# Kernel optimization log

Hardware: AMD Instinct MI355X
Metric: run time of the kernel (lower is better)

The kernel has to match this reference:

```python
import jax, jax.numpy as jnp
import numpy as np
from jax import lax

B, C, H, W = 8, 128, 48, 48
N = H * W
SPARSITY = 0.8
K_TOP = int(N * SPARSITY)


def conv2d(x, w, b, padding, dilation=1):
    # x: [B,C,H,W], w: [O,I,kh,kw]
    out = lax.conv_general_dilated(
        x, w, window_strides=(1, 1),
        padding=[(padding, padding), (padding, padding)],
        rhs_dilation=(dilation, dilation),
        dimension_numbers=('NCHW', 'OIHW', 'NCHW'))
    return out + b[None, :, None, None]


def setup_inputs() -> dict:
    key = jax.random.key(0)
    ks = jax.random.split(key, 16)
    s = 0.02
    return {
        'x': jax.random.normal(ks[0], (B, C, H, W), jnp.float32),
        'prev_features': jax.random.normal(ks[1], (B, C, H, W), jnp.float32),
        'Wq': jax.random.normal(ks[2], (C, C), jnp.float32) * s,
        'bq': jnp.zeros((C,), jnp.float32),
        'Wk': jax.random.normal(ks[3], (C, C), jnp.float32) * s,
        'bk': jnp.zeros((C,), jnp.float32),
        'Wv': jax.random.normal(ks[4], (C, C), jnp.float32) * s,
        'bv': jnp.zeros((C,), jnp.float32),
        'ref_w': jax.random.normal(ks[5], (C, C, 3, 3), jnp.float32) * s,
        'ref_b': jnp.zeros((C,), jnp.float32),
        'gate_w': jax.random.normal(ks[6], (1, C, 3, 3), jnp.float32) * s,
        'gate_b': jnp.zeros((1,), jnp.float32),
        'cov_w': jax.random.normal(ks[7], (C, C, 3, 3), jnp.float32) * s,
        'cov_b': jnp.zeros((C,), jnp.float32),
    }


def reference(x, prev_features, Wq, bq, Wk, bk, Wv, bv,
              ref_w, ref_b, gate_w, gate_b, cov_w, cov_b):
    b_, c_, h_, w_ = x.shape
    n_ = h_ * w_
    # torch x.view(B, -1, C): raw reshape of NCHW memory (NOT a transpose)
    t = x.reshape(b_, n_, c_)
    # Linear layers (torch: y = x @ W.T + b)
    Q = t @ Wq.T + bq
    Kt = (t @ Wk.T + bk).transpose(0, 2, 1)  # [B,C,N]
    V = t @ Wv.T + bv
    attn = jnp.einsum('bnc,bcm->bnm', Q, Kt) / (c_ ** 0.5)  # [B,N,N]
    # top-k masking with scatter, as in the original
    _, idx = lax.top_k(attn, K_TOP)  # [B,N,k]
    bi = jnp.arange(b_)[:, None, None]
    ni = jnp.arange(n_)[None, :, None]
    mask = jnp.zeros_like(attn).at[bi, ni, idx].set(1.0)
    attn = attn * mask - 1e10 * (1.0 - mask)
    attn = jax.nn.softmax(attn, axis=-1)
    out = jnp.einsum('bnm,bmc->bnc', attn, V)  # [B,N,C]
    # torch view([B, C, sqrt(N), sqrt(N)]): raw reshape
    xs = out.reshape(b_, c_, h_, w_)
    # localized refinement
    importance = jax.nn.sigmoid(conv2d(xs, gate_w, gate_b, padding=1))
    xr = conv2d(xs * importance, ref_w, ref_b, padding=1)
    xs = xs + xr
    # temporal propagation
    xs = xs + 0.5 * prev_features
    # fast coverage conv: kernel 3, dilation 2, padding = 1 + 2 - 1 = 2
    return conv2d(xs, cov_w, cov_b, padding=2, dilation=2)
```

## Files before the change

kernel.cpp:

```cpp
#include <hip/hip_runtime.h>
#include <hip/hip_bf16.h>
#include <math.h>

#define BB 8
#define CC 128
#define NTOK 2304
#define KTOP 1843

typedef unsigned short u16;
typedef unsigned int   u32;
typedef __attribute__((ext_vector_type(8))) short short8;
typedef __attribute__((ext_vector_type(4))) float f32x4;

static __device__ __forceinline__ float bf2f(u16 u) {
    return __uint_as_float(((u32)u) << 16);
}
static __device__ __forceinline__ u16 f2bf(float f) {
    u32 x = __float_as_uint(f);
    return (u16)((x + 0x7fffu + ((x >> 16) & 1u)) >> 16);
}

__global__ __launch_bounds__(256) void qkv_kernel(
    const float* __restrict__ x,
    const float* __restrict__ Wq, const float* __restrict__ bq,
    const float* __restrict__ Wk, const float* __restrict__ bk,
    const float* __restrict__ Wv, const float* __restrict__ bv,
    u16* __restrict__ q_ws, u16* __restrict__ k_ws, u16* __restrict__ v_ws)
{
    __shared__ float t_lds[128 * 68];
    __shared__ u16 st[64 * 128];
    int blk = blockIdx.x;
    int b  = blk / 36;
    int n0 = (blk % 36) * 64;
    int tid = threadIdx.x;
    const float* xb = x + (size_t)(b * NTOK + n0) * CC;
    #pragma unroll
    for (int k = 0; k < 32; ++k) {
        int idx = k * 256 + tid;
        t_lds[(idx & 127) * 68 + (idx >> 7)] = xb[idx];
    }
    __syncthreads();
    int o  = tid & 127;
    int rh = tid >> 7;
    const float* Ws[3] = {Wq, Wk, Wv};
    const float* bs[3] = {bq, bk, bv};
    for (int mat = 0; mat < 3; ++mat) {
        const float* W = Ws[mat];
        float acc[32];
        #pragma unroll
        for (int j = 0; j < 32; ++j) acc[j] = 0.f;
        for (int c = 0; c < 128; ++c) {
            float w = W[o * 128 + c];
            const float4* t4p = (const float4*)&t_lds[c * 68 + rh * 32];
            #pragma unroll
            for (int j4 = 0; j4 < 8; ++j4) {
                float4 t4 = t4p[j4];
                acc[j4*4+0] += t4.x * w;
                acc[j4*4+1] += t4.y * w;
                acc[j4*4+2] += t4.z * w;
                acc[j4*4+3] += t4.w * w;
            }
        }
        float bias = bs[mat][o];
        if (mat == 2) {
            ushort4* vp4 = (ushort4*)(v_ws + (size_t)(b * CC + o) * NTOK + n0 + rh * 32);
            #pragma unroll
            for (int j8 = 0; j8 < 8; ++j8) {
                ushort4 s;
                s.x = f2bf(acc[j8*4+0] + bias); s.y = f2bf(acc[j8*4+1] + bias);
                s.z = f2bf(acc[j8*4+2] + bias); s.w = f2bf(acc[j8*4+3] + bias);
                vp4[j8] = s;
            }
        } else {
            #pragma unroll
            for (int j = 0; j < 32; ++j)
                st[(rh * 32 + j) * 128 + o] = f2bf(acc[j] + bias);
            __syncthreads();
            u16* gp = (mat == 0 ? q_ws : k_ws) + (size_t)(b * NTOK + n0) * CC;
            const ushort4* s4 = (const ushort4*)st;
            ushort4* g4 = (ushort4*)gp;
            for (int k = tid; k < 2048; k += 256) g4[k] = s4[k];
            __syncthreads();
        }
    }
}

__global__ __launch_bounds__(512) void attn_kernel(
    const u16* __restrict__ q_ws, const u16* __restrict__ k_ws,
    const u16* __restrict__ v_ws, float* __restrict__ xs_ws)
{
    __shared__ u16 sp[16 * NTOK];
    __shared__ float rowinv[16];
    int tid  = threadIdx.x;
    int lane = tid & 63, wid = tid >> 6;
    int b  = blockIdx.x & 7;
    int n0 = (blockIdx.x >> 3) * 16;
    const float scale = 0.08838834764831845f;

    int fr = lane & 15;
    int fg = lane >> 4;

    const u16* qbase = q_ws + (size_t)(b * NTOK + n0 + fr) * CC + fg * 8;
    short8 qa[4];
    #pragma unroll
    for (int kc = 0; kc < 4; ++kc)
        qa[kc] = *(const short8*)(qbase + kc * 32);

    const u16* kb = k_ws + (size_t)(b * NTOK + fr) * CC + fg * 8;
    for (int t = wid; t < 144; t += 8) {
        int m0 = t * 16;
        f32x4 acc = {0.f, 0.f, 0.f, 0.f};
        const u16* kp = kb + (size_t)m0 * CC;
        #pragma unroll
        for (int kc = 0; kc < 4; ++kc) {
            short8 kf = *(const short8*)(kp + kc * 32);
            acc = __builtin_amdgcn_mfma_f32_16x16x32_bf16(qa[kc], kf, acc, 0, 0, 0);
        }
        int mcol = m0 + fr;
        #pragma unroll
        for (int r = 0; r < 4; ++r) {
            int q = fg * 4 + r;
            sp[q * NTOK + (mcol ^ ((q & 7) << 3))] = f2bf(acc[r] * scale);
        }
    }
    __syncthreads();

    for (int rr = 0; rr < 2; ++rr) {
        int row = wid * 2 + rr;
        int xorv = (row & 7) << 3;
        u16* srow = sp + row * NTOK;
        int keys[36];
        float vmax = -1e30f;
        #pragma unroll
        for (int j = 0; j < 36; ++j) {
            int m = lane + j * 64;
            u16 raw = srow[m ^ xorv];
            u32 key = (raw & 0x8000u) ? (u32)(0xFFFFu & ~(u32)raw) : (u32)(raw | 0x8000u);
            keys[j] = (int)key;
            vmax = fmaxf(vmax, bf2f(raw));
        }
        #pragma unroll
        for (int off = 32; off; off >>= 1) vmax = fmaxf(vmax, __shfl_xor(vmax, off, 64));
        u32 res = 0;
        for (int bit = 15; bit >= 0; --bit) {
            int cand = (int)(res | (1u << bit));
            int cnt = 0;
            #pragma unroll
            for (int j = 0; j < 36; ++j) cnt += (keys[j] >= cand) ? 1 : 0;
            #pragma unroll
            for (int off = 32; off; off >>= 1) cnt += __shfl_xor(cnt, off, 64);
            if (cnt >= KTOP) res = (u32)cand;
        }
        float lsum = 0.f;
        #pragma unroll
        for (int j = 0; j < 36; ++j) {
            int m = lane + j * 64;
            float e = 0.f;
            if ((u32)keys[j] >= res) e = __expf(bf2f(srow[m ^ xorv]) - vmax);
            srow[m ^ xorv] = f2bf(e);
            lsum += e;
        }
        #pragma unroll
        for (int off = 32; off; off >>= 1) lsum += __shfl_xor(lsum, off, 64);
        if (lane == 0) rowinv[row] = 1.f / lsum;
    }
    __syncthreads();

    {
        int c0 = wid * 16;
        const u16* vb = v_ws + (size_t)(b * CC + c0 + fr) * NTOK + fg * 8;
        const u16* arow = sp + fr * NTOK;
        int xorv = (fr & 7) << 3;
        f32x4 oacc = {0.f, 0.f, 0.f, 0.f};
        for (int ch = 0; ch < 72; ++ch) {
            int m0 = ch * 32;
            short8 pa = *(const short8*)(arow + ((m0 + fg * 8) ^ xorv));
            short8 vf = *(const short8*)(vb + m0);
            oacc = __builtin_amdgcn_mfma_f32_16x16x32_bf16(pa, vf, oacc, 0, 0, 0);
        }
        #pragma unroll
        for (int r = 0; r < 4; ++r) {
            int q = fg * 4 + r;
            xs_ws[(size_t)(b * NTOK + n0 + q) * CC + c0 + fr] = oacc[r] * rowinv[q];
        }
    }
}

__global__ __launch_bounds__(256) void gate_kernel(
    const float* __restrict__ xs_ws, const float* __restrict__ gw,
    const float* __restrict__ gb, float* __restrict__ imp_ws)
{
    __shared__ float gsum[256];
    int blk = blockIdx.x;
    int b  = blk & 7;
    int p0 = (blk >> 3) * 64;
    int tid = threadIdx.x;
    int pl = tid & 63, cq = tid >> 6;
    int p = p0 + pl;
    int h = p / 48, w = p % 48;
    float acc = 0.f;
    const float* xb = xs_ws + (size_t)b * CC * NTOK;
    for (int i = cq * 32; i < cq * 32 + 32; ++i) {
        const float* plane = xb + (size_t)i * NTOK;
        const float* wv = gw + i * 9;
        #pragma unroll
        for (int kh = 0; kh < 3; ++kh) {
            int hh = h + kh - 1;
            if ((unsigned)hh >= 48u) continue;
            #pragma unroll
            for (int kw = 0; kw < 3; ++kw) {
                int ww = w + kw - 1;
                if ((unsigned)ww >= 48u) continue;
                acc += plane[hh * 48 + ww] * wv[kh * 3 + kw];
            }
        }
    }
    gsum[cq * 64 + pl] = acc;
    __syncthreads();
    if (tid < 64) {
        float s = gsum[tid] + gsum[64 + tid] + gsum[128 + tid] + gsum[192 + tid] + gb[0];
        imp_ws[b * NTOK + p0 + tid] = 1.f / (1.f + __expf(-s));
    }
}

__global__ __launch_bounds__(256) void wtrans_kernel(
    const float* __restrict__ rw, const float* __restrict__ cw,
    u16* __restrict__ wb_ref, u16* __restrict__ wb_cov)
{
    int idx = blockIdx.x * 256 + threadIdx.x;
    int which = idx >= 147456;
    int rem = which ? idx - 147456 : idx;
    int tap = rem >> 14;
    int rest = rem & 16383;
    int o = rest >> 7, c = rest & 127;
    const float* src = which ? cw : rw;
    u16* dst = which ? wb_cov : wb_ref;
    dst[rem] = f2bf(src[(o * 128 + c) * 9 + tap]);
}

__global__ __launch_bounds__(256) void tpos_kernel(
    const float* __restrict__ xs_ws, const float* __restrict__ prev,
    const float* __restrict__ imp_ws,
    u16* __restrict__ xt_g, float* __restrict__ rbuf)
{
    __shared__ float tx[128 * 65];
    __shared__ float tp[128 * 65];
    int blk = blockIdx.x;
    int b  = blk & 7;
    int p0 = (blk >> 3) * 64;
    int tid = threadIdx.x;
    const float* xsb = xs_ws + (size_t)b * CC * NTOK + p0;
    const float* pvb = prev  + (size_t)b * CC * NTOK + p0;
    #pragma unroll
    for (int it = 0; it < 32; ++it) {
        int idx = it * 256 + tid;
        int i = idx >> 6, pp = idx & 63;
        tx[i * 65 + pp] = xsb[(size_t)i * NTOK + pp];
        tp[i * 65 + pp] = pvb[(size_t)i * NTOK + pp];
    }
    __syncthreads();
    int pl = tid & 63, cq = tid >> 6;
    float impv = imp_ws[b * NTOK + p0 + pl];
    size_t obase = ((size_t)b * NTOK + p0 + pl) * CC + cq * 32;
    u16* gout = xt_g + obase;
    float* rout = rbuf + obase;
    #pragma unroll
    for (int j4 = 0; j4 < 8; ++j4) {
        float4 rv; ushort4 gv;
        float v0 = tx[(cq * 32 + j4 * 4 + 0) * 65 + pl];
        float v1 = tx[(cq * 32 + j4 * 4 + 1) * 65 + pl];
        float v2 = tx[(cq * 32 + j4 * 4 + 2) * 65 + pl];
        float v3 = tx[(cq * 32 + j4 * 4 + 3) * 65 + pl];
        float q0 = tp[(cq * 32 + j4 * 4 + 0) * 65 + pl];
        float q1 = tp[(cq * 32 + j4 * 4 + 1) * 65 + pl];
        float q2 = tp[(cq * 32 + j4 * 4 + 2) * 65 + pl];
        float q3 = tp[(cq * 32 + j4 * 4 + 3) * 65 + pl];
        rv.x = v0 + 0.5f * q0; rv.y = v1 + 0.5f * q1;
        rv.z = v2 + 0.5f * q2; rv.w = v3 + 0.5f * q3;
        gv.x = f2bf(v0 * impv); gv.y = f2bf(v1 * impv);
        gv.z = f2bf(v2 * impv); gv.w = f2bf(v3 * impv);
        *(float4*)(rout + j4 * 4) = rv;
        *(ushort4*)(gout + j4 * 4) = gv;
    }
}

__global__ __launch_bounds__(256) void refgemm_kernel(
    const u16* __restrict__ xt_g, const u16* __restrict__ wb_ref,
    const float* __restrict__ rbuf, const float* __restrict__ rb,
    u16* __restrict__ xt2)
{
    __shared__ u16 slab[144 * 128];
    int tid = threadIdx.x;
    int lane = tid & 63, wid = tid >> 6;
    int blk = blockIdx.x;
    int b  = blk & 7;
    int st = (blk >> 3) & 15;
    int oh = blk >> 7;
    int h0 = st * 3;
    int p0g = st * 144;
    int fr = lane & 15, fg = lane >> 4;
    int o0 = oh * 64 + wid * 16;
    const u16* xb = xt_g + (size_t)b * NTOK * CC;

    f32x4 acc[9];
    #pragma unroll
    for (int pt = 0; pt < 9; ++pt) acc[pt] = (f32x4){0.f, 0.f, 0.f, 0.f};

    for (int tap = 0; tap < 9; ++tap) {
        int dh = tap / 3 - 1, dw = tap % 3 - 1;
        __syncthreads();
        #pragma unroll
        for (int it = 0; it < 9; ++it) {
            int idx = it * 256 + tid;
            int pr = idx >> 4, cv = idx & 15;
            int r = pr >= 96 ? 2 : (pr >= 48 ? 1 : 0);
            int w = pr - r * 48;
            int sh = h0 + r + dh, sw = w + dw;
            short8 val = (short8){0,0,0,0,0,0,0,0};
            if ((unsigned)sh < 48u && (unsigned)sw < 48u)
                val = *(const short8*)(xb + (size_t)(sh * 48 + sw) * CC + cv * 8);
            *(short8*)(slab + pr * 128 + ((cv ^ (pr & 7)) * 8)) = val;
        }
        __syncthreads();
        #pragma unroll
        for (int kc = 0; kc < 4; ++kc) {
            short8 bfr = *(const short8*)(wb_ref + tap * 16384 + (o0 + fr) * 128 + kc * 32 + fg * 8);
            #pragma unroll
            for (int pt = 0; pt < 9; ++pt) {
                int prr = pt * 16 + fr;
                short8 pa = *(const short8*)(slab + prr * 128 + (((kc * 4 + fg) ^ (prr & 7)) * 8));
                acc[pt] = __builtin_amdgcn_mfma_f32_16x16x32_bf16(pa, bfr, acc[pt], 0, 0, 0);
            }
        }
    }
    int o = o0 + fr;
    float bias = rb[o];
    #pragma unroll
    for (int pt = 0; pt < 9; ++pt) {
        #pragma unroll
        for (int r = 0; r < 4; ++r) {
            int p = p0g + pt * 16 + fg * 4 + r;
            size_t off = ((size_t)b * NTOK + p) * CC + o;
            float v = acc[pt][r] + bias + rbuf[off];
            xt2[off] = f2bf(v);
        }
    }
}

__global__ __launch_bounds__(256) void covgemm_kernel(
    const u16* __restrict__ xt2, const u16* __restrict__ wb_cov,
    const float* __restrict__ cb, float* __restrict__ out)
{
    __shared__ u16 slab[144 * 128];
    __shared__ float ldsout[4 * 16 * 145];
    int tid = threadIdx.x;
    int lane = tid & 63, wid = tid >> 6;
    int blk = blockIdx.x;
    int b  = blk & 7;
    int st = (blk >> 3) & 15;
    int oh = blk >> 7;
    int h0 = st * 3;
    int p0g = st * 144;
    int fr = lane & 15, fg = lane >> 4;
    int o0 = oh * 64 + wid * 16;
    const u16* xb = xt2 + (size_t)b * NTOK * CC;

    f32x4 acc[9];
    #pragma unroll
    for (int pt = 0; pt < 9; ++pt) acc[pt] = (f32x4){0.f, 0.f, 0.f, 0.f};

    for (int tap = 0; tap < 9; ++tap) {
        int dh = (tap / 3 - 1) * 2, dw = (tap % 3 - 1) * 2;
        __syncthreads();
        #pragma unroll
        for (int it = 0; it < 9; ++it) {
            int idx = it * 256 + tid;
            int pr = idx >> 4, cv = idx & 15;
            int r = pr >= 96 ? 2 : (pr >= 48 ? 1 : 0);
            int w = pr - r * 48;
            int sh = h0 + r + dh, sw = w + dw;
            short8 val = (short8){0,0,0,0,0,0,0,0};
            if ((unsigned)sh < 48u && (unsigned)sw < 48u)
                val = *(const short8*)(xb + (size_t)(sh * 48 + sw) * CC + cv * 8);
            *(short8*)(slab + pr * 128 + ((cv ^ (pr & 7)) * 8)) = val;
        }
        __syncthreads();
        #pragma unroll
        for (int kc = 0; kc < 4; ++kc) {
            short8 bfr = *(const short8*)(wb_cov + tap * 16384 + (o0 + fr) * 128 + kc * 32 + fg * 8);
            #pragma unroll
            for (int pt = 0; pt < 9; ++pt) {
                int prr = pt * 16 + fr;
                short8 pa = *(const short8*)(slab + prr * 128 + (((kc * 4 + fg) ^ (prr & 7)) * 8));
                acc[pt] = __builtin_amdgcn_mfma_f32_16x16x32_bf16(pa, bfr, acc[pt], 0, 0, 0);
            }
        }
    }
    float bias = cb[o0 + fr];
    float* lo = ldsout + wid * (16 * 145);
    #pragma unroll
    for (int pt = 0; pt < 9; ++pt) {
        #pragma unroll
        for (int r = 0; r < 4; ++r) {
            int pl = pt * 16 + fg * 4 + r;
            lo[fr * 145 + pl] = acc[pt][r] + bias;
        }
    }
    __syncthreads();
    float* ob = out + ((size_t)b * CC + o0) * NTOK + p0g;
    #pragma unroll
    for (int j = 0; j < 36; ++j) {
        int idx = j * 64 + lane;
        int o_r = idx / 144;
        int p_r = idx - o_r * 144;
        ob[(size_t)o_r * NTOK + p_r] = lo[o_r * 145 + p_r];
    }
}

extern "C" void kernel_launch(void* const* d_in, const int* in_sizes, int n_in,
                              void* d_out, int out_size, void* d_ws, size_t ws_size,
                              hipStream_t stream)
{
    const float* x    = (const float*)d_in[0];
    const float* prev = (const float*)d_in[1];
    const float* Wq   = (const float*)d_in[2];
    const float* bq   = (const float*)d_in[3];
    const float* Wk   = (const float*)d_in[4];
    const float* bk   = (const float*)d_in[5];
    const float* Wv   = (const float*)d_in[6];
    const float* bv   = (const float*)d_in[7];
    const float* rw   = (const float*)d_in[8];
    const float* rb   = (const float*)d_in[9];
    const float* gw   = (const float*)d_in[10];
    const float* gb   = (const float*)d_in[11];
    const float* cw   = (const float*)d_in[12];
    const float* cb   = (const float*)d_in[13];
    float* out = (float*)d_out;
    char* ws = (char*)d_ws;

    const size_t SZ  = (size_t)BB * NTOK * CC;
    const size_t BSZ = SZ * 2;
    const size_t FSZ = SZ * 4;
    u16*   q_ws   = (u16*)(ws);
    u16*   k_ws   = (u16*)(ws + BSZ);
    u16*   v_ws   = (u16*)(ws + 2 * BSZ);
    float* xs_ws  = (float*)(ws + 3 * BSZ);
    float* imp_ws = (float*)(ws + 3 * BSZ + FSZ);
    u16*   xt_g   = (u16*)(ws + 3 * BSZ + FSZ + 73728);
    float* rbuf   = (float*)(ws + 4 * BSZ + FSZ + 73728);
    u16*   xt2    = (u16*)(ws + 4 * BSZ + 2 * FSZ + 73728);
    u16*   wb_ref = (u16*)(ws + 5 * BSZ + 2 * FSZ + 73728);
    u16*   wb_cov = (u16*)(ws + 5 * BSZ + 2 * FSZ + 73728 + 294912);

    qkv_kernel<<<dim3(288), dim3(256), 0, stream>>>(x, Wq, bq, Wk, bk, Wv, bv,
                                                    q_ws, k_ws, v_ws);
    attn_kernel<<<dim3(1152), dim3(512), 0, stream>>>(q_ws, k_ws, v_ws, xs_ws);
    gate_kernel<<<dim3(288), dim3(256), 0, stream>>>(xs_ws, gw, gb, imp_ws);
    wtrans_kernel<<<dim3(1152), dim3(256), 0, stream>>>(rw, cw, wb_ref, wb_cov);
    tpos_kernel<<<dim3(288), dim3(256), 0, stream>>>(xs_ws, prev, imp_ws, xt_g, rbuf);
    refgemm_kernel<<<dim3(256), dim3(256), 0, stream>>>(xt_g, wb_ref, rbuf, rb, xt2);
    covgemm_kernel<<<dim3(256), dim3(256), 0, stream>>>(xt2, wb_cov, cb, out);
}
```

Before: 586.5 us.

## Shrink attention tiles to 8 query rows, store sort keys, fold scale into Q

Attention blocks now cover 8 query rows with 4 waves instead of 16 rows with 8 waves, halving shared memory per block and doubling the grid. Score tiles are stored directly as monotone sort keys so the top-k pass needs no conversion, and the max is taken on keys. The softmax scale is folded into Q in the QKV kernel. Each wave handles two rows at once for ILP and two V column tiles per MFMA loop. The cost is that half of each 16-row MFMA output is wasted on duplicate rows.

Result: slower. 656.2 us (+11.9%).

```diff
diff --git a/kernel.cpp b/kernel.cpp
--- a/kernel.cpp
+++ b/kernel.cpp
@@ -18,6 +18,10 @@
 static __device__ __forceinline__ u16 f2bf(float f) {
     u32 x = __float_as_uint(f);
     return (u16)((x + 0x7fffu + ((x >> 16) & 1u)) >> 16);
+}
+static __device__ __forceinline__ float key2val(int k) {
+    u32 raw = (k & 0x8000) ? (u32)(k ^ 0x8000) : ((~(u32)k) & 0xFFFFu);
+    return __uint_as_float(raw << 16);
 }
 
 __global__ __launch_bounds__(256) void qkv_kernel(
@@ -72,9 +76,10 @@
                 vp4[j8] = s;
             }
         } else {
+            float sc = (mat == 0) ? 0.08838834764831845f : 1.0f;
             #pragma unroll
             for (int j = 0; j < 32; ++j)
-                st[(rh * 32 + j) * 128 + o] = f2bf(acc[j] + bias);
+                st[(rh * 32 + j) * 128 + o] = f2bf((acc[j] + bias) * sc);
             __syncthreads();
             u16* gp = (mat == 0 ? q_ws : k_ws) + (size_t)(b * NTOK + n0) * CC;
             const ushort4* s4 = (const ushort4*)st;
@@ -85,29 +90,27 @@
     }
 }
 
-__global__ __launch_bounds__(512) void attn_kernel(
+__global__ __launch_bounds__(256) void attn_kernel(
     const u16* __restrict__ q_ws, const u16* __restrict__ k_ws,
     const u16* __restrict__ v_ws, float* __restrict__ xs_ws)
 {
-    __shared__ u16 sp[16 * NTOK];
-    __shared__ float rowinv[16];
+    __shared__ u16 sp[8 * NTOK];
+    __shared__ float rowinv[8];
     int tid  = threadIdx.x;
     int lane = tid & 63, wid = tid >> 6;
     int b  = blockIdx.x & 7;
-    int n0 = (blockIdx.x >> 3) * 16;
-    const float scale = 0.08838834764831845f;
-
+    int n0 = (blockIdx.x >> 3) * 8;
     int fr = lane & 15;
     int fg = lane >> 4;
 
-    const u16* qbase = q_ws + (size_t)(b * NTOK + n0 + fr) * CC + fg * 8;
+    const u16* qbase = q_ws + (size_t)(b * NTOK + n0 + (fr & 7)) * CC + fg * 8;
     short8 qa[4];
     #pragma unroll
     for (int kc = 0; kc < 4; ++kc)
         qa[kc] = *(const short8*)(qbase + kc * 32);
 
     const u16* kb = k_ws + (size_t)(b * NTOK + fr) * CC + fg * 8;
-    for (int t = wid; t < 144; t += 8) {
+    for (int t = wid; t < 144; t += 4) {
         int m0 = t * 16;
         f32x4 acc = {0.f, 0.f, 0.f, 0.f};
         const u16* kp = kb + (size_t)m0 * CC;
@@ -116,72 +119,106 @@
             short8 kf = *(const short8*)(kp + kc * 32);
             acc = __builtin_amdgcn_mfma_f32_16x16x32_bf16(qa[kc], kf, acc, 0, 0, 0);
         }
-        int mcol = m0 + fr;
-        #pragma unroll
-        for (int r = 0; r < 4; ++r) {
-            int q = fg * 4 + r;
-            sp[q * NTOK + (mcol ^ ((q & 7) << 3))] = f2bf(acc[r] * scale);
+        if (fg < 2) {
+            int mcol = m0 + fr;
+            #pragma unroll
+            for (int r = 0; r < 4; ++r) {
+                int q = fg * 4 + r;
+                u16 raw = f2bf(acc[r]);
+                u16 key = (raw & 0x8000u) ? (u16)~raw : (u16)(raw | 0x8000u);
+                sp[q * NTOK + (mcol ^ ((q & 7) << 3))] = key;
+            }
         }
     }
     __syncthreads();
 
-    for (int rr = 0; rr < 2; ++rr) {
-        int row = wid * 2 + rr;
-        int xorv = (row & 7) << 3;
-        u16* srow = sp + row * NTOK;
-        int keys[36];
-        float vmax = -1e30f;
+    {
+        int row0 = wid * 2, row1 = row0 + 1;
+        int x0 = (row0 & 7) << 3, x1 = (row1 & 7) << 3;
+        u16* s0 = sp + row0 * NTOK;
+        u16* s1 = sp + row1 * NTOK;
+        int keys0[36], keys1[36];
+        int kmax0 = 0, kmax1 = 0;
         #pragma unroll
         for (int j = 0; j < 36; ++j) {
             int m = lane + j * 64;
-            u16 raw = srow[m ^ xorv];
-            u32 key = (raw & 0x8000u) ? (u32)(0xFFFFu & ~(u32)raw) : (u32)(raw | 0x8000u);
-            keys[j] = (int)key;
-            vmax = fmaxf(vmax, bf2f(raw));
-        }
-        #pragma unroll
-        for (int off = 32; off; off >>= 1) vmax = fmaxf(vmax, __shfl_xor(vmax, off, 64));
-        u32 res = 0;
+            int k0 = s0[m ^ x0];
+            int k1 = s1[m ^ x1];
+            keys0[j] = k0; keys1[j] = k1;
+            kmax0 = max(kmax0, k0); kmax1 = max(kmax1, k1);
+        }
+        #pragma unroll
+        for (int off = 32; off; off >>= 1) {
+            kmax0 = max(kmax0, __shfl_xor(kmax0, off, 64));
+            kmax1 = max(kmax1, __shfl_xor(kmax1, off, 64));
+        }
+        u32 res0 = 0, res1 = 0;
         for (int bit = 15; bit >= 0; --bit) {
-            int cand = (int)(res | (1u << bit));
-            int cnt = 0;
-            #pragma unroll
-            for (int j = 0; j < 36; ++j) cnt += (keys[j] >= cand) ? 1 : 0;
-            #pragma unroll
-            for (int off = 32; off; off >>= 1) cnt += __shfl_xor(cnt, off, 64);
-            if (cnt >= KTOP) res = (u32)cand;
-        }
-        float lsum = 0.f;
+            int cand0 = (int)(res0 | (1u << bit));
+            int cand1 = (int)(res1 | (1u << bit));
+            int c0 = 0, c1 = 0;
+            #pragma unroll
+            for (int j = 0; j < 36; ++j) {
+                c0 += (keys0[j] >= cand0) ? 1 : 0;
+                c1 += (keys1[j] >= cand1) ? 1 : 0;
+            }
+            #pragma unroll
+            for (int off = 32; off; off >>= 1) {
+                c0 += __shfl_xor(c0, off, 64);
+                c1 += __shfl_xor(c1, off, 64);
+            }
+            if (c0 >= KTOP) res0 = (u32)cand0;
+            if (c1 >= KTOP) res1 = (u32)cand1;
+        }
+        float vmax0 = key2val(kmax0), vmax1 = key2val(kmax1);
+        float sum0 = 0.f, sum1 = 0.f;
         #pragma unroll
         for (int j = 0; j < 36; ++j) {
             int m = lane + j * 64;
-            float e = 0.f;
-            if ((u32)keys[j] >= res) e = __expf(bf2f(srow[m ^ xorv]) - vmax);
-            srow[m ^ xorv] = f2bf(e);
-            lsum += e;
-        }
-        #pragma unroll
-        for (int off = 32; off; off >>= 1) lsum += __shfl_xor(lsum, off, 64);
-        if (lane == 0) rowinv[row] = 1.f / lsum;
+            float e0 = 0.f, e1 = 0.f;
+            if ((u32)keys0[j] >= res0) e0 = __expf(key2val(keys0[j]) - vmax0);
+            if ((u32)keys1[j] >= res1) e1 = __expf(key2val(keys1[j]) - vmax1);
+            s0[m ^ x0] = f2bf(e0);
+            s1[m ^ x1] = f2bf(e1);
+            sum0 += e0; sum1 += e1;
+        }
+        #pragma unroll
+        for (int off = 32; off; off >>= 1) {
+            sum0 += __shfl_xor(sum0, off, 64);
+            sum1 += __shfl_xor(sum1, off, 64);
+        }
+        if (lane == 0) {
+            rowinv[row0] = 1.f / sum0;
+            rowinv[row1] = 1.f / sum1;
+        }
     }
     __syncthreads();
 
     {
-        int c0 = wid * 16;
-        const u16* vb = v_ws + (size_t)(b * CC + c0 + fr) * NTOK + fg * 8;
-        const u16* arow = sp + fr * NTOK;
+        int c0 = wid * 32;
+        const u16* arow = sp + (fr & 7) * NTOK;
         int xorv = (fr & 7) << 3;
-        f32x4 oacc = {0.f, 0.f, 0.f, 0.f};
+        const u16* vb0 = v_ws + (size_t)(b * CC + c0 + fr) * NTOK + fg * 8;
+        const u16* vb1 = vb0 + (size_t)16 * NTOK;
+        f32x4 oa = {0.f, 0.f, 0.f, 0.f};
+        f32x4 ob = {0.f, 0.f, 0.f, 0.f};
         for (int ch = 0; ch < 72; ++ch) {
             int m0 = ch * 32;
             short8 pa = *(const short8*)(arow + ((m0 + fg * 8) ^ xorv));
-            short8 vf = *(const short8*)(vb + m0);
-            oacc = __builtin_amdgcn_mfma_f32_16x16x32_bf16(pa, vf, oacc, 0, 0, 0);
-        }
-        #pragma unroll
-        for (int r = 0; r < 4; ++r) {
-            int q = fg * 4 + r;
-            xs_ws[(size_t)(b * NTOK + n0 + q) * CC + c0 + fr] = oacc[r] * rowinv[q];
+            short8 v0 = *(const short8*)(vb0 + m0);
+            short8 v1 = *(const short8*)(vb1 + m0);
+            oa = __builtin_amdgcn_mfma_f32_16x16x32_bf16(pa, v0, oa, 0, 0, 0);
+            ob = __builtin_amdgcn_mfma_f32_16x16x32_bf16(pa, v1, ob, 0, 0, 0);
+        }
+        if (fg < 2) {
+            #pragma unroll
+            for (int r = 0; r < 4; ++r) {
+                int q = fg * 4 + r;
+                float inv = rowinv[q];
+                size_t base = (size_t)(b * NTOK + n0 + q) * CC + c0;
+                xs_ws[base + fr]      = oa[r] * inv;
+                xs_ws[base + 16 + fr] = ob[r] * inv;
+            }
         }
     }
 }
@@ -454,7 +491,7 @@
 
     qkv_kernel<<<dim3(288), dim3(256), 0, stream>>>(x, Wq, bq, Wk, bk, Wv, bv,
                                                     q_ws, k_ws, v_ws);
-    attn_kernel<<<dim3(1152), dim3(512), 0, stream>>>(q_ws, k_ws, v_ws, xs_ws);
+    attn_kernel<<<dim3(2304), dim3(256), 0, stream>>>(q_ws, k_ws, v_ws, xs_ws);
     gate_kernel<<<dim3(288), dim3(256), 0, stream>>>(xs_ws, gw, gb, imp_ws);
     wtrans_kernel<<<dim3(1152), dim3(256), 0, stream>>>(rw, cw, wb_ref, wb_cov);
     tpos_kernel<<<dim3(288), dim3(256), 0, stream>>>(xs_ws, prev, imp_ws, xt_g, rbuf);
```
